# Performance work log

Measured on AMD Instinct MI355X. Metric: run time of the kernel, lower is better.

## Reference

```python
import jax, jax.numpy as jnp
import numpy as np
from jax import lax

# Module config (matches init_kwargs)
IN_DIM = 1
OUT_DIM = 64
TMIN_MS, TMAX_MS, FS = 0, 500, 128
LIMIT = 7.0            # limitOfShift_idx
N_BASIS = 21
MAX_N = N_BASIS // 2   # 10
# msec2Idxs([0,500],128) -> arange(0, 64+1); nWin=65
LAG_IDXS = np.arange(int(round(TMIN_MS / 1000.0 * FS)), int(round(TMAX_MS / 1000.0 * FS)) + 1)
N_WIN = len(LAG_IDXS)                 # 65
N_LAG = N_WIN + 2 * int(LIMIT)        # 79 (extended TRF support)
T_PERIOD = float(N_LAG - 1)           # 78, Fourier basis period

BATCH, N_SEQ = 8, 4096


def setup_inputs() -> dict:
    key = jax.random.key(0)
    k1, k2, k3, k4 = jax.random.split(key, 4)
    x = jax.random.normal(k1, (BATCH, IN_DIM, N_SEQ), dtype=jnp.float32)
    conv_w = jax.random.normal(k2, (3, IN_DIM, 2), dtype=jnp.float32) * 0.5   # Conv1d(inDim, 3, kernel=2)
    conv_b = jax.random.normal(k3, (3,), dtype=jnp.float32) * 0.1
    coefs = jax.random.normal(k4, (OUT_DIM, IN_DIM, N_BASIS), dtype=jnp.float32)
    return {"x": x, "conv_w": conv_w, "conv_b": conv_b, "coefs": coefs}


def reference(x, conv_w, conv_b, coefs):
    # --- CausalConv: left-pad by (k-1)=1 then valid conv ---
    xp = jnp.pad(x, ((0, 0), (0, 0), (1, 0)))
    params = lax.conv_general_dilated(
        xp, conv_w, window_strides=(1,), padding='VALID',
        dimension_numbers=('NCH', 'OIH', 'NCH')) + conv_b[None, :, None]
    # params: (batch, 3, nSeq) -> warp params a, b, c
    a = jnp.abs(params[:, 0])                         # (b, s) gain
    bshift = jnp.clip(params[:, 1], -LIMIT, LIMIT)    # (b, s) lag shift
    c = jnp.clip(1.0 + params[:, 2], 0.5, 1.4)        # (b, s) time dilation

    lag = jnp.arange(N_WIN, dtype=x.dtype) + LIMIT            # lagIdxs + limit, (w,)
    t = c[:, None, :] * (lag[None, :, None] - bshift[:, None, :])   # (b, w, s)

    # --- FourierBasisTRF.vecFourierSum ---
    seqN = jnp.arange(1, MAX_N + 1, dtype=x.dtype)            # (maxN,)
    ang = (2.0 * jnp.pi / T_PERIOD) * t[..., None] * seqN     # (b, w, s, maxN)
    scale = 1.0 / jnp.sqrt(T_PERIOD / 2.0)
    # interleave sin/cos: [sin1, cos1, sin2, cos2, ...]
    constN = (jnp.stack([jnp.sin(ang), jnp.cos(ang)], axis=-1)
              .reshape(*ang.shape[:3], 2 * MAX_N)) * scale    # (b, w, s, 2*maxN)
    const0 = 1.0 / (jnp.sqrt(2.0) * jnp.sqrt(T_PERIOD / 2.0))

    # out[b,o,i,w,s] = const0*coefs[o,i,0] + sum_n constN[b,w,s,n]*coefs[o,i,1+n]
    out = (const0 * coefs[:, :, 0])[None, :, :, None, None] \
        + jnp.einsum('bwsn,oin->boiws', constN, coefs[:, :, 1:])

    # gain and sum over input-channel axis (axis 2)
    trfs = (a[:, None, None, None, :] * out).sum(axis=2)      # (b, outDim, nWin, nSeq)
    return trfs
```

## Files before the change

kernel.cpp:

```cpp
#include <hip/hip_runtime.h>
#include <math.h>

#define BATCH 8
#define NSEQ  4096
#define NWIN  65
#define OUTD  64
#define NB    21

typedef __attribute__((ext_vector_type(4))) float f32x4;

__global__ __launch_bounds__(256, 4) void trf_kernel(
    const float* __restrict__ x,
    const float* __restrict__ conv_w,
    const float* __restrict__ conv_b,
    const float* __restrict__ coefs,
    float* __restrict__ out)
{
    const int tid   = threadIdx.x;
    const int blk   = blockIdx.x;
    const int og    = blk & 3;
    const int chunk = (blk >> 2) & 3;
    const int bw    = blk >> 4;
    const int w     = bw % NWIN;
    const int b     = bw / NWIN;
    const int s0    = chunk * 1024 + tid * 4;

    const float w00 = conv_w[0], w01 = conv_w[1];
    const float w10 = conv_w[2], w11 = conv_w[3];
    const float w20 = conv_w[4], w21 = conv_w[5];
    const float cb0 = conv_b[0], cb1 = conv_b[1], cb2 = conv_b[2];

    const float* xb = x + (size_t)b * NSEQ;
    const f32x4 xq  = *(const f32x4*)(xb + s0);
    const float xm0 = (s0 > 0) ? xb[s0 - 1] : 0.0f;

    const float K      = 0.08055365778435367f;
    const float SCALE  = 0.16012815380508713f;
    const float CONST0 = 0.11322770341445958f;
    const float wl     = (float)(w + 7);

    f32x4 basis[NB];
#pragma unroll
    for (int p = 0; p < 4; ++p) {
        const float xm = (p == 0) ? xm0 : xq[p - 1];
        const float xc = xq[p];
        const float p0 = fmaf(xm, w00, fmaf(xc, w01, cb0));
        const float p1 = fmaf(xm, w10, fmaf(xc, w11, cb1));
        const float p2 = fmaf(xm, w20, fmaf(xc, w21, cb2));
        const float a  = fabsf(p0);
        const float bs = fminf(fmaxf(p1, -7.0f), 7.0f);
        const float c  = fminf(fmaxf(1.0f + p2, 0.5f), 1.4f);

        const float theta = K * c * (wl - bs);
        float sn, cn;
        __sincosf(theta, &sn, &cn);

        const float fa = a * SCALE;
        basis[0][p] = a * CONST0;
        const float twoc = 2.0f * cn;
        float sp = 0.0f, cp = 1.0f;
        float scur = sn, ccur = cn;
#pragma unroll
        for (int n = 1; n <= 10; ++n) {
            basis[2 * n - 1][p] = fa * scur;
            basis[2 * n][p]     = fa * ccur;
            const float snew = fmaf(twoc, scur, -sp);
            const float cnew = fmaf(twoc, ccur, -cp);
            sp = scur; cp = ccur; scur = snew; ccur = cnew;
        }
    }

    float* op = out + ((size_t)(b * OUTD + og * 16) * NWIN + (size_t)w) * NSEQ + s0;
    const size_t ostride = (size_t)NWIN * NSEQ;

    const float* cwb = coefs + og * 16 * NB;
    f32x4 acc[4];
#pragma unroll
    for (int j = 0; j < 16; ++j) {
        const float* cw = cwb + j * NB;
        f32x4 a0 = basis[0] * cw[0];
#pragma unroll
        for (int n = 1; n < NB; ++n) {
            const float cs = cw[n];
            const f32x4 cv = {cs, cs, cs, cs};
            a0 = __builtin_elementwise_fma(basis[n], cv, a0);
        }
        acc[j & 3] = a0;
        __builtin_nontemporal_store(acc[j & 3], (f32x4*)(op + (size_t)j * ostride));
    }
}

extern "C" void kernel_launch(void* const* d_in, const int* in_sizes, int n_in,
                              void* d_out, int out_size, void* d_ws, size_t ws_size,
                              hipStream_t stream) {
    const float* x      = (const float*)d_in[0];
    const float* conv_w = (const float*)d_in[1];
    const float* conv_b = (const float*)d_in[2];
    const float* coefs  = (const float*)d_in[3];
    float* out = (float*)d_out;

    const int blocks = BATCH * NWIN * 4  * 4 ;
    trf_kernel<<<blocks, 256, 0, stream>>>(x, conv_w, conv_b, coefs, out);
}
```

Baseline: 97.26 us.

## Compute coefficient contraction with bf16 MFMA via LDS-staged basis tiles

Replaces the per-thread FMA contraction over 21 basis terms with a 16x16x32 bf16 MFMA. Each wave computes basis values per sequence position, packs them as bf16 into LDS, and multiplies them against a bf16 coefficient fragment. The goal is to cut VALU work. In exchange it adds LDS traffic, lowers precision to bf16, which may break tolerance, and replaces 16-byte stores with scalar 4-byte stores, which weakens store coalescing on an output-bandwidth-bound kernel.

```diff
diff --git a/kernel.cpp b/kernel.cpp
--- a/kernel.cpp
+++ b/kernel.cpp
@@ -8,6 +8,14 @@
 #define NB    21
 
 typedef __attribute__((ext_vector_type(4))) float f32x4;
+typedef __attribute__((ext_vector_type(4))) int   i32x4;
+typedef __attribute__((ext_vector_type(8))) short bf16x8;
+
+static __device__ __forceinline__ unsigned int f2bf(float f) {
+    unsigned int u = __builtin_bit_cast(unsigned int, f);
+    u += 0x7fffu + ((u >> 16) & 1u);
+    return u >> 16;
+}
 
 __global__ __launch_bounds__(256, 4) void trf_kernel(
     const float* __restrict__ x,
@@ -16,77 +24,124 @@
     const float* __restrict__ coefs,
     float* __restrict__ out)
 {
-    const int tid   = threadIdx.x;
-    const int blk   = blockIdx.x;
+    const int tid  = threadIdx.x;
+    const int lane = tid & 63;
+    const int wid  = tid >> 6;
+    const int blk  = blockIdx.x;
     const int og    = blk & 3;
     const int chunk = (blk >> 2) & 3;
     const int bw    = blk >> 4;
     const int w     = bw % NWIN;
     const int b     = bw / NWIN;
-    const int s0    = chunk * 1024 + tid * 4;
+
+    __shared__ int lds_i[4 * 128 * 20];
 
     const float w00 = conv_w[0], w01 = conv_w[1];
     const float w10 = conv_w[2], w11 = conv_w[3];
     const float w20 = conv_w[4], w21 = conv_w[5];
     const float cb0 = conv_b[0], cb1 = conv_b[1], cb2 = conv_b[2];
 
-    const float* xb = x + (size_t)b * NSEQ;
-    const f32x4 xq  = *(const f32x4*)(xb + s0);
-    const float xm0 = (s0 > 0) ? xb[s0 - 1] : 0.0f;
-
     const float K      = 0.08055365778435367f;
     const float SCALE  = 0.16012815380508713f;
     const float CONST0 = 0.11322770341445958f;
     const float wl     = (float)(w + 7);
 
-    f32x4 basis[NB];
+    const int col  = lane & 15;
+    const int kseg = lane >> 4;
+
+    const int o_row = og * 16 + col;
+    unsigned int au0, au1, au2, au3;
+    {
+        const float* cr = coefs + o_row * NB;
+        float f[8];
 #pragma unroll
-    for (int p = 0; p < 4; ++p) {
-        const float xm = (p == 0) ? xm0 : xq[p - 1];
-        const float xc = xq[p];
-        const float p0 = fmaf(xm, w00, fmaf(xc, w01, cb0));
-        const float p1 = fmaf(xm, w10, fmaf(xc, w11, cb1));
-        const float p2 = fmaf(xm, w20, fmaf(xc, w21, cb2));
-        const float a  = fabsf(p0);
-        const float bs = fminf(fmaxf(p1, -7.0f), 7.0f);
-        const float c  = fminf(fmaxf(1.0f + p2, 0.5f), 1.4f);
+        for (int e = 0; e < 8; ++e) {
+            const int k = kseg * 8 + e;
+            f[e] = (k < NB) ? cr[k] : 0.0f;
+        }
+        au0 = f2bf(f[0]) | (f2bf(f[1]) << 16);
+        au1 = f2bf(f[2]) | (f2bf(f[3]) << 16);
+        au2 = f2bf(f[4]) | (f2bf(f[5]) << 16);
+        au3 = f2bf(f[6]) | (f2bf(f[7]) << 16);
+    }
+    const bf16x8 afrag = __builtin_bit_cast(bf16x8,
+        (i32x4){(int)au0, (int)au1, (int)au2, (int)au3});
 
-        const float theta = K * c * (wl - bs);
-        float sn, cn;
-        __sincosf(theta, &sn, &cn);
+    const float* xb = x + (size_t)b * NSEQ;
+    const int s_wave = chunk * 1024 + wid * 256;
 
-        const float fa = a * SCALE;
-        basis[0][p] = a * CONST0;
-        const float twoc = 2.0f * cn;
-        float sp = 0.0f, cp = 1.0f;
-        float scur = sn, ccur = cn;
+    const size_t PL = (size_t)NWIN * NSEQ;
+    float* o_base = out
+        + ((size_t)(b * OUTD + og * 16 + kseg * 4) * NWIN + (size_t)w) * NSEQ
+        + s_wave + col;
+
+    int* const lds_w = &lds_i[wid * (128 * 20)];
+
 #pragma unroll
-        for (int n = 1; n <= 10; ++n) {
-            basis[2 * n - 1][p] = fa * scur;
-            basis[2 * n][p]     = fa * ccur;
-            const float snew = fmaf(twoc, scur, -sp);
-            const float cnew = fmaf(twoc, ccur, -cp);
-            sp = scur; cp = ccur; scur = snew; ccur = cnew;
+    for (int h = 0; h < 2; ++h) {
+        asm volatile("s_waitcnt lgkmcnt(0)" ::: "memory");
+        __builtin_amdgcn_sched_barrier(0);
+
+#pragma unroll
+        for (int pp = 0; pp < 2; ++pp) {
+            const int q     = lane + 64 * pp;
+            const int s_idx = s_wave + h * 128 + q;
+            const float xc = xb[s_idx];
+            const float xm = (s_idx > 0) ? xb[s_idx - 1] : 0.0f;
+
+            const float p0 = fmaf(xm, w00, fmaf(xc, w01, cb0));
+            const float p1 = fmaf(xm, w10, fmaf(xc, w11, cb1));
+            const float p2 = fmaf(xm, w20, fmaf(xc, w21, cb2));
+            const float a  = fabsf(p0);
+            const float bs = fminf(fmaxf(p1, -7.0f), 7.0f);
+            const float c  = fminf(fmaxf(1.0f + p2, 0.5f), 1.4f);
+
+            const float theta = K * c * (wl - bs);
+            float sn, cn;
+            __sincosf(theta, &sn, &cn);
+
+            float bas[NB];
+            const float fa = a * SCALE;
+            bas[0] = a * CONST0;
+            const float twoc = 2.0f * cn;
+            float sp = 0.0f, cp = 1.0f;
+            float scur = sn, ccur = cn;
+#pragma unroll
+            for (int n = 1; n <= 10; ++n) {
+                bas[2 * n - 1] = fa * scur;
+                bas[2 * n]     = fa * ccur;
+                const float snew = fmaf(twoc, scur, -sp);
+                const float cnew = fmaf(twoc, ccur, -cp);
+                sp = scur; cp = ccur; scur = snew; ccur = cnew;
+            }
+
+            unsigned int u[11];
+#pragma unroll
+            for (int i = 0; i < 10; ++i)
+                u[i] = f2bf(bas[2 * i]) | (f2bf(bas[2 * i + 1]) << 16);
+            u[10] = f2bf(bas[20]);
+
+            int* row = lds_w + q * 20;
+            *(i32x4*)(row)      = (i32x4){(int)u[0], (int)u[1], (int)u[2], (int)u[3]};
+            *(i32x4*)(row + 4)  = (i32x4){(int)u[4], (int)u[5], (int)u[6], (int)u[7]};
+            *(i32x4*)(row + 8)  = (i32x4){(int)u[8], (int)u[9], (int)u[10], 0};
+            *(i32x4*)(row + 12) = (i32x4){0, 0, 0, 0};
         }
-    }
 
-    float* op = out + ((size_t)(b * OUTD + og * 16) * NWIN + (size_t)w) * NSEQ + s0;
-    const size_t ostride = (size_t)NWIN * NSEQ;
+        asm volatile("s_waitcnt lgkmcnt(0)" ::: "memory");
+        __builtin_amdgcn_sched_barrier(0);
 
-    const float* cwb = coefs + og * 16 * NB;
-    f32x4 acc[4];
 #pragma unroll
-    for (int j = 0; j < 16; ++j) {
-        const float* cw = cwb + j * NB;
-        f32x4 a0 = basis[0] * cw[0];
+        for (int t = 0; t < 8; ++t) {
+            const i32x4 bi = *(const i32x4*)(lds_w + (t * 16 + col) * 20 + kseg * 4);
+            const bf16x8 bfrag = __builtin_bit_cast(bf16x8, bi);
+            const f32x4 d = __builtin_amdgcn_mfma_f32_16x16x32_bf16(
+                afrag, bfrag, (f32x4){0.f, 0.f, 0.f, 0.f}, 0, 0, 0);
+            const int soff = h * 128 + t * 16;
 #pragma unroll
-        for (int n = 1; n < NB; ++n) {
-            const float cs = cw[n];
-            const f32x4 cv = {cs, cs, cs, cs};
-            a0 = __builtin_elementwise_fma(basis[n], cv, a0);
+            for (int r = 0; r < 4; ++r)
+                __builtin_nontemporal_store(d[r], o_base + (size_t)r * PL + soff);
         }
-        acc[j & 3] = a0;
-        __builtin_nontemporal_store(acc[j & 3], (f32x4*)(op + (size_t)j * ostride));
     }
 }
 
```

New measurement: 165.1 us. 1.7x slower.
